# Performance work log

Measured on AMD Instinct MI355X. Metric: run time of the kernel, lower is better.

Reference implementation:

```python
import jax, jax.numpy as jnp
import numpy as np

E, K, H, I, T, CAP = 32, 4, 2048, 2048, 512, 256
ALPHA, LIMIT = 1.702, 7.0


def _dyn_quant(x):
    # symmetric per-token int8 dynamic quant (npu_dynamic_quant): dequant = q * scale
    s = jnp.max(jnp.abs(x), axis=-1, keepdims=True) / 127.0
    q = jnp.clip(jnp.round(x / s), -127.0, 127.0)  # int8 values kept in f32 for exact-emulated GEMM
    return q, jnp.squeeze(s, -1)


def _swiglu(x):
    glu = jnp.minimum(x[..., ::2], LIMIT)          # interleaved layout, upper clamp only
    lin = jnp.clip(x[..., 1::2], -LIMIT, LIMIT)
    return glu * jax.nn.sigmoid(ALPHA * glu) * (lin + 1.0)


def _forward(hidden_states, router_logits, gate_up_proj, gate_up_proj_scale,
             gate_up_proj_bias, down_proj, down_proj_scale, down_proj_bias):
    # --- gating: softmax + top-k, renormalize weights (npu_moe_gating_top_k + explicit renorm) ---
    probs = jax.nn.softmax(router_logits, axis=-1)
    topk_w, topk_ids = jax.lax.top_k(probs, K)                     # [T,K]
    topk_w = topk_w / jnp.sum(topk_w, axis=-1, keepdims=True)
    # --- per-token dynamic int8 quant of activations ---
    q_x, x_scale = _dyn_quant(hidden_states)                        # [T,H], [T]
    # --- capacity-based dispatch (emulates npu_moe_init_routing_v2 sort/scatter) ---
    flat_e = topk_ids.reshape(-1)                                   # [T*K]
    tok = jnp.repeat(jnp.arange(T), K)
    oh = jax.nn.one_hot(flat_e, E, dtype=jnp.int32)
    pos = jnp.take_along_axis(jnp.cumsum(oh, axis=0) - 1, flat_e[:, None], axis=1)[:, 0]
    valid = pos < CAP
    x_disp = jnp.zeros((E, CAP, H), jnp.float32).at[flat_e, pos].set(q_x[tok], mode='drop')
    s_disp = jnp.zeros((E, CAP), jnp.float32).at[flat_e, pos].set(x_scale[tok], mode='drop')
    gu = jnp.einsum('ech,ehf->ecf', x_disp, gate_up_proj.astype(jnp.float32))
    gu = gu * s_disp[:, :, None] * gate_up_proj_scale[:, None, :] + gate_up_proj_bias[:, None, :]
    act = _swiglu(gu)                                               # [E,CAP,I]
    # --- requantize + grouped GEMM 2 + bias ---
    q2, s2 = _dyn_quant(act)
    dn = jnp.einsum('eci,eio->eco', q2, down_proj.astype(jnp.float32))
    dn = dn * s2[:, :, None] * down_proj_scale[:, None, :] + down_proj_bias[:, None, :]
    # --- finalize routing: gather back and weighted combine ---
    pos_c = jnp.minimum(pos, CAP - 1)
    y = dn[flat_e, pos_c] * valid[:, None].astype(jnp.float32)      # [T*K,H]
    return jnp.sum(y.reshape(T, K, H) * topk_w[:, :, None], axis=1)


def setup_inputs() -> dict:
    key = jax.random.key(0)
    k = jax.random.split(key, 8)
    hidden_states = jax.random.normal(k[0], (T, H), jnp.float32)
    router_logits = jax.random.normal(k[1], (T, E), jnp.float32)
    gate_up_proj = jax.random.randint(k[2], (E, H, 2 * I), -127, 128, jnp.int32).astype(jnp.int8)
    w_s = float(2.0 / (127.0 * np.sqrt(H)))
    gate_up_proj_scale = (0.5 + 0.5 * jax.random.uniform(k[3], (E, 2 * I), jnp.float32)) * w_s
    gate_up_proj_bias = 0.02 * jax.random.normal(k[4], (E, 2 * I), jnp.float32)
    down_proj = jax.random.randint(k[5], (E, I, H), -127, 128, jnp.int32).astype(jnp.int8)
    d_s = float(2.0 / (127.0 * np.sqrt(I)))
    down_proj_scale = (0.5 + 0.5 * jax.random.uniform(k[6], (E, H), jnp.float32)) * d_s
    down_proj_bias = 0.02 * jax.random.normal(k[7], (E, H), jnp.float32)
    return dict(hidden_states=hidden_states, router_logits=router_logits,
                gate_up_proj=gate_up_proj, gate_up_proj_scale=gate_up_proj_scale,
                gate_up_proj_bias=gate_up_proj_bias, down_proj=down_proj,
                down_proj_scale=down_proj_scale, down_proj_bias=down_proj_bias)


def reference(hidden_states, router_logits, gate_up_proj, gate_up_proj_scale,
              gate_up_proj_bias, down_proj, down_proj_scale, down_proj_bias):
    return _forward(hidden_states, router_logits, gate_up_proj, gate_up_proj_scale,
                    gate_up_proj_bias, down_proj, down_proj_scale, down_proj_bias)
```

## Files before the change

### kernel.cpp

```cpp
#include <hip/hip_runtime.h>
#include <hip/hip_bf16.h>
#include <math.h>

constexpr int E_EXP = 32;
constexpr int TOPK  = 4;
constexpr int H_DIM = 2048;
constexpr int I_DIM = 2048;
constexpr int T_TOK = 512;
constexpr int CAP   = 256;
constexpr int TWOI  = 4096;
constexpr int NPAIR = T_TOK * TOPK;
constexpr float ALPHA = 1.702f;
constexpr float LIMIT = 7.0f;


typedef int v4i  __attribute__((ext_vector_type(4)));
typedef int v16i __attribute__((ext_vector_type(16)));

__device__ __forceinline__ float waveReduceMax(float v) {
    #pragma unroll
    for (int off = 32; off > 0; off >>= 1)
        v = fmaxf(v, __shfl_xor(v, off, 64));
    return v;
}

__global__ void k_router(const float* __restrict__ logits,
                         int* __restrict__ topk_ids,
                         float* __restrict__ topk_w) {
    int t = blockIdx.x * blockDim.x + threadIdx.x;
    if (t >= T_TOK) return;
    float l[E_EXP];
    float mx = -1e30f;
    #pragma unroll
    for (int e = 0; e < E_EXP; e++) { l[e] = logits[t * E_EXP + e]; mx = fmaxf(mx, l[e]); }
    #pragma unroll
    for (int e = 0; e < E_EXP; e++) { l[e] = expf(l[e] - mx); }

    float v[TOPK]; int id[TOPK];
    #pragma unroll
    for (int k = 0; k < TOPK; k++) {
        float best = -1.0f; int bi = 0;
        #pragma unroll
        for (int e = 0; e < E_EXP; e++) {
            bool taken = false;
            for (int j = 0; j < k; j++) taken = taken || (id[j] == e);
            if (!taken && l[e] > best) { best = l[e]; bi = e; }
        }
        v[k] = best; id[k] = bi;
    }
    float inv = 1.0f / (v[0] + v[1] + v[2] + v[3]);
    #pragma unroll
    for (int k = 0; k < TOPK; k++) {
        topk_ids[t * TOPK + k] = id[k];
        topk_w[t * TOPK + k]   = v[k] * inv;
    }
}

__global__ void k_quant_x(const float* __restrict__ x,
                          signed char* __restrict__ qx,
                          float* __restrict__ xs) {
    int t = blockIdx.x, tid = threadIdx.x;
    const float4* xr = (const float4*)(x + (size_t)t * H_DIM);
    float4 v0 = xr[tid * 2], v1 = xr[tid * 2 + 1];
    float am = fmaxf(fmaxf(fmaxf(fabsf(v0.x), fabsf(v0.y)), fmaxf(fabsf(v0.z), fabsf(v0.w))),
                     fmaxf(fmaxf(fabsf(v1.x), fabsf(v1.y)), fmaxf(fabsf(v1.z), fabsf(v1.w))));
    __shared__ float red[4];
    am = waveReduceMax(am);
    if ((tid & 63) == 0) red[tid >> 6] = am;
    __syncthreads();
    am = fmaxf(fmaxf(red[0], red[1]), fmaxf(red[2], red[3]));
    float s = am * (1.0f / 127.0f);
    if (tid == 0) xs[t] = s;
    float vv[8] = {v0.x, v0.y, v0.z, v0.w, v1.x, v1.y, v1.z, v1.w};
    int out[2]; signed char* ob = (signed char*)out;
    #pragma unroll
    for (int j = 0; j < 8; j++) {
        float q = (s > 0.f) ? rintf(vv[j] / s) : 0.f;
        q = fminf(127.f, fmaxf(-127.f, q));
        ob[j] = (signed char)q;
    }
    ((int2*)(qx + (size_t)t * H_DIM))[tid] = *(int2*)out;
}

__global__ void k_dispatch(const int* __restrict__ topk_ids,
                           int* __restrict__ pair_pos,
                           int* __restrict__ rows_map,
                           int* __restrict__ counts) {
    int e = blockIdx.x;
    int lane = threadIdx.x;
    int base = 0;
    unsigned long long lt = (1ull << lane) - 1ull;
    if (lane == 63) lt = 0x7FFFFFFFFFFFFFFFull;
    for (int i0 = 0; i0 < NPAIR; i0 += 64) {
        int idx = i0 + lane;
        int ee = topk_ids[idx];
        bool m = (ee == e);
        unsigned long long mask = __ballot(m);
        int pre = __popcll(mask & lt);
        if (m) {
            int pos = base + pre;
            pair_pos[idx] = pos;
            if (pos < CAP) rows_map[e * CAP + pos] = idx;
        }
        base += __popcll(mask);
    }
    if (lane == 0) counts[e] = (base < CAP) ? base : CAP;
}

__global__ void k_scan(const int* __restrict__ counts, int* __restrict__ offs) {
    if (threadIdx.x == 0 && blockIdx.x == 0) {
        int a = 0;
        for (int e = 0; e < E_EXP; e++) { offs[e] = a; a += counts[e]; }
        offs[E_EXP] = a;
    }
}

#define MT 128
#define NT 64
#define KC 64
#define LSTR 80

__global__ __launch_bounds__(256, 4) void k_gemm1(
    const signed char* __restrict__ qx, const float* __restrict__ xs,
    const int* __restrict__ W, const float* __restrict__ wscale,
    const float* __restrict__ wbias, const int* __restrict__ rows_map,
    const int* __restrict__ counts, const int* __restrict__ offs,
    float* __restrict__ act) {
    int e = blockIdx.z;
    int cnt = counts[e];
    int m0 = blockIdx.y * MT;
    if (m0 >= cnt) return;
    int rb = offs[e];
    int n0 = blockIdx.x * NT;
    int tid = threadIdx.x;

    __shared__ __align__(16) signed char a_lds[MT * LSTR];
    __shared__ __align__(16) signed char b_lds[NT * LSTR];
    __shared__ int   asrc_lds[MT];
    __shared__ float s_lds[MT];

    if (tid < MT) {
        int r = m0 + tid;
        int tok = 0; float sc = 0.f;
        if (r < cnt) { int pair = rows_map[e * CAP + r]; tok = pair >> 2; sc = xs[tok]; }
        asrc_lds[tid] = tok; s_lds[tid] = sc;
    }
    __syncthreads();

    int arow = tid >> 2, ahalf = tid & 3;
    const signed char* ap0 = qx + (size_t)asrc_lds[arow]      * H_DIM + ahalf * 16;
    const signed char* ap1 = qx + (size_t)asrc_lds[arow + 64] * H_DIM + ahalf * 16;
    signed char* aw0 = a_lds + arow * LSTR + ahalf * 16;
    signed char* aw1 = a_lds + (arow + 64) * LSTR + ahalf * 16;

    int nq = tid & 15, kq = tid >> 4;
    const int* bp = W + (size_t)e * H_DIM * TWOI + (size_t)(kq * 4) * TWOI + n0 + nq * 4;
    int* bw = (int*)(b_lds + (nq * 4) * LSTR) + kq;

    int lane = tid & 63, wv = tid >> 6;
    int wr = wv >> 1, wc = wv & 1;
    int l31 = lane & 31, lhi = lane >> 5;
    const signed char* ar = a_lds + (wr * 64 + l31) * LSTR + lhi * 16;
    const signed char* br = b_lds + (wc * 32 + l31) * LSTR + lhi * 16;

    v16i acc0 = {}, acc1 = {};

    for (int k0 = 0; k0 < H_DIM; k0 += KC) {
        int4 va0 = *(const int4*)ap0;
        int4 va1 = *(const int4*)ap1;
        int4 w0 = *(const int4*)(bp);
        int4 w1 = *(const int4*)(bp + TWOI);
        int4 w2 = *(const int4*)(bp + 2 * TWOI);
        int4 w3 = *(const int4*)(bp + 3 * TWOI);
        ap0 += KC; ap1 += KC; bp += (size_t)KC * TWOI;

        *(int4*)aw0 = va0;
        *(int4*)aw1 = va1;
        bw[0]      = (w0.x & 255) | ((w1.x & 255) << 8) | ((w2.x & 255) << 16) | (w3.x << 24);
        bw[20]     = (w0.y & 255) | ((w1.y & 255) << 8) | ((w2.y & 255) << 16) | (w3.y << 24);
        bw[40]     = (w0.z & 255) | ((w1.z & 255) << 8) | ((w2.z & 255) << 16) | (w3.z << 24);
        bw[60]     = (w0.w & 255) | ((w1.w & 255) << 8) | ((w2.w & 255) << 16) | (w3.w << 24);
        __syncthreads();

        #pragma unroll
        for (int kk = 0; kk < 2; kk++) {
            v4i bf = *(const v4i*)(br + kk * 32);
            v4i a0 = *(const v4i*)(ar + kk * 32);
            v4i a1 = *(const v4i*)(ar + 32 * LSTR + kk * 32);
            acc0 = __builtin_amdgcn_mfma_i32_32x32x32_i8(a0, bf, acc0, 0, 0, 0);
            acc1 = __builtin_amdgcn_mfma_i32_32x32x32_i8(a1, bf, acc1, 0, 0, 0);
        }
        __syncthreads();
    }

    int c = n0 + wc * 32 + l31;
    float wsc = wscale[e * TWOI + c];
    float wbs = wbias[e * TWOI + c];
    bool evenc = (l31 & 1) == 0;
    #pragma unroll
    for (int i = 0; i < 2; i++) {
        #pragma unroll
        for (int reg = 0; reg < 16; reg++) {
            int row_local = wr * 64 + i * 32 + (reg & 3) + 8 * (reg >> 2) + 4 * lhi;
            int accv = (i == 0) ? acc0[reg] : acc1[reg];
            float val = (float)accv * s_lds[row_local] * wsc + wbs;
            float other = __shfl_xor(val, 1, 64);
            int r = m0 + row_local;
            if (evenc && r < cnt) {
                float g   = fminf(val, LIMIT);
                float lin = fminf(fmaxf(other, -LIMIT), LIMIT);
                float sig = 1.0f / (1.0f + expf(-ALPHA * g));
                act[(size_t)(rb + r) * I_DIM + (c >> 1)] = g * sig * (lin + 1.0f);
            }
        }
    }
}

__global__ void k_quant_act(const float* __restrict__ act,
                            const int* __restrict__ counts,
                            const int* __restrict__ offs,
                            signed char* __restrict__ aq,
                            float* __restrict__ as_) {
    int e = blockIdx.x / CAP, p = blockIdx.x % CAP;
    if (p >= counts[e]) return;
    int row = offs[e] + p;
    int tid = threadIdx.x;
    const float4* xr = (const float4*)(act + (size_t)row * I_DIM);
    float4 v0 = xr[tid * 2], v1 = xr[tid * 2 + 1];
    float am = fmaxf(fmaxf(fmaxf(fabsf(v0.x), fabsf(v0.y)), fmaxf(fabsf(v0.z), fabsf(v0.w))),
                     fmaxf(fmaxf(fabsf(v1.x), fabsf(v1.y)), fmaxf(fabsf(v1.z), fabsf(v1.w))));
    __shared__ float red[4];
    am = waveReduceMax(am);
    if ((tid & 63) == 0) red[tid >> 6] = am;
    __syncthreads();
    am = fmaxf(fmaxf(red[0], red[1]), fmaxf(red[2], red[3]));
    float s = am * (1.0f / 127.0f);
    if (tid == 0) as_[row] = s;
    float vv[8] = {v0.x, v0.y, v0.z, v0.w, v1.x, v1.y, v1.z, v1.w};
    int out[2]; signed char* ob = (signed char*)out;
    #pragma unroll
    for (int j = 0; j < 8; j++) {
        float q = (s > 0.f) ? rintf(vv[j] / s) : 0.f;
        q = fminf(127.f, fmaxf(-127.f, q));
        ob[j] = (signed char)q;
    }
    ((int2*)(aq + (size_t)row * I_DIM))[tid] = *(int2*)out;
}

__global__ __launch_bounds__(256, 4) void k_gemm2(
    const signed char* __restrict__ aq, const float* __restrict__ as_,
    const int* __restrict__ W, const float* __restrict__ wscale,
    const float* __restrict__ wbias, const int* __restrict__ rows_map,
    const int* __restrict__ counts, const int* __restrict__ offs,
    float* __restrict__ dn_rows) {
    int e = blockIdx.z;
    int cnt = counts[e];
    int m0 = blockIdx.y * MT;
    if (m0 >= cnt) return;
    int rb = offs[e];
    int n0 = blockIdx.x * NT;
    int tid = threadIdx.x;

    __shared__ __align__(16) signed char a_lds[MT * LSTR];
    __shared__ __align__(16) signed char b_lds[NT * LSTR];
    __shared__ int   asrc_lds[MT];
    __shared__ int   pair_lds[MT];
    __shared__ float s_lds[MT];

    if (tid < MT) {
        int r = m0 + tid;
        int src = rb; int pr = 0; float sc = 0.f;
        if (r < cnt) { src = rb + r; pr = rows_map[e * CAP + r]; sc = as_[rb + r]; }
        asrc_lds[tid] = src; pair_lds[tid] = pr; s_lds[tid] = sc;
    }
    __syncthreads();

    int arow = tid >> 2, ahalf = tid & 3;
    const signed char* ap0 = aq + (size_t)asrc_lds[arow]      * I_DIM + ahalf * 16;
    const signed char* ap1 = aq + (size_t)asrc_lds[arow + 64] * I_DIM + ahalf * 16;
    signed char* aw0 = a_lds + arow * LSTR + ahalf * 16;
    signed char* aw1 = a_lds + (arow + 64) * LSTR + ahalf * 16;

    int nq = tid & 15, kq = tid >> 4;
    const int* bp = W + (size_t)e * I_DIM * H_DIM + (size_t)(kq * 4) * H_DIM + n0 + nq * 4;
    int* bw = (int*)(b_lds + (nq * 4) * LSTR) + kq;

    int lane = tid & 63, wv = tid >> 6;
    int wr = wv >> 1, wc = wv & 1;
    int l31 = lane & 31, lhi = lane >> 5;
    const signed char* ar = a_lds + (wr * 64 + l31) * LSTR + lhi * 16;
    const signed char* br = b_lds + (wc * 32 + l31) * LSTR + lhi * 16;

    v16i acc0 = {}, acc1 = {};

    for (int k0 = 0; k0 < I_DIM; k0 += KC) {
        int4 va0 = *(const int4*)ap0;
        int4 va1 = *(const int4*)ap1;
        int4 w0 = *(const int4*)(bp);
        int4 w1 = *(const int4*)(bp + H_DIM);
        int4 w2 = *(const int4*)(bp + 2 * H_DIM);
        int4 w3 = *(const int4*)(bp + 3 * H_DIM);
        ap0 += KC; ap1 += KC; bp += (size_t)KC * H_DIM;

        *(int4*)aw0 = va0;
        *(int4*)aw1 = va1;
        bw[0]  = (w0.x & 255) | ((w1.x & 255) << 8) | ((w2.x & 255) << 16) | (w3.x << 24);
        bw[20] = (w0.y & 255) | ((w1.y & 255) << 8) | ((w2.y & 255) << 16) | (w3.y << 24);
        bw[40] = (w0.z & 255) | ((w1.z & 255) << 8) | ((w2.z & 255) << 16) | (w3.z << 24);
        bw[60] = (w0.w & 255) | ((w1.w & 255) << 8) | ((w2.w & 255) << 16) | (w3.w << 24);
        __syncthreads();

        #pragma unroll
        for (int kk = 0; kk < 2; kk++) {
            v4i bf = *(const v4i*)(br + kk * 32);
            v4i a0 = *(const v4i*)(ar + kk * 32);
            v4i a1 = *(const v4i*)(ar + 32 * LSTR + kk * 32);
            acc0 = __builtin_amdgcn_mfma_i32_32x32x32_i8(a0, bf, acc0, 0, 0, 0);
            acc1 = __builtin_amdgcn_mfma_i32_32x32x32_i8(a1, bf, acc1, 0, 0, 0);
        }
        __syncthreads();
    }

    int c = n0 + wc * 32 + l31;
    float wsc = wscale[e * H_DIM + c];
    float wbs = wbias[e * H_DIM + c];
    #pragma unroll
    for (int i = 0; i < 2; i++) {
        #pragma unroll
        for (int reg = 0; reg < 16; reg++) {
            int row_local = wr * 64 + i * 32 + (reg & 3) + 8 * (reg >> 2) + 4 * lhi;
            int r = m0 + row_local;
            if (r < cnt) {
                int accv = (i == 0) ? acc0[reg] : acc1[reg];
                float val = (float)accv * s_lds[row_local] * wsc + wbs;
                dn_rows[(size_t)pair_lds[row_local] * H_DIM + c] = val;
            }
        }
    }
}

__global__ void k_finalize(const float* __restrict__ dn_rows,
                           const float* __restrict__ topk_w,
                           const int* __restrict__ pair_pos,
                           float* __restrict__ out) {
    int t = blockIdx.x, tid = threadIdx.x;
    int h = tid * 8;
    float acc[8] = {0, 0, 0, 0, 0, 0, 0, 0};
    #pragma unroll
    for (int k = 0; k < TOPK; k++) {
        int pair = t * TOPK + k;
        if (pair_pos[pair] < CAP) {
            float w = topk_w[pair];
            const float4* dr = (const float4*)(dn_rows + (size_t)pair * H_DIM + h);
            float4 d0 = dr[0], d1 = dr[1];
            acc[0] += w * d0.x; acc[1] += w * d0.y; acc[2] += w * d0.z; acc[3] += w * d0.w;
            acc[4] += w * d1.x; acc[5] += w * d1.y; acc[6] += w * d1.z; acc[7] += w * d1.w;
        }
    }
    float4* o = (float4*)(out + (size_t)t * H_DIM + h);
    o[0] = make_float4(acc[0], acc[1], acc[2], acc[3]);
    o[1] = make_float4(acc[4], acc[5], acc[6], acc[7]);
}

extern "C" void kernel_launch(void* const* d_in, const int* in_sizes, int n_in,
                              void* d_out, int out_size, void* d_ws, size_t ws_size,
                              hipStream_t stream) {
    const float* hidden  = (const float*)d_in[0];
    const float* rlogits = (const float*)d_in[1];
    const int*   gup     = (const int*)d_in[2];
    const float* gup_s   = (const float*)d_in[3];
    const float* gup_b   = (const float*)d_in[4];
    const int*   dnw     = (const int*)d_in[5];
    const float* dn_s    = (const float*)d_in[6];
    const float* dn_b    = (const float*)d_in[7];
    float*       out     = (float*)d_out;

    char* ws = (char*)d_ws;
    size_t off = 0;
    auto alloc = [&](size_t bytes) -> void* {
        void* p = ws + off;
        off = (off + bytes + 255) & ~(size_t)255;
        return p;
    };
    signed char* qx       = (signed char*)alloc((size_t)T_TOK * H_DIM);
    float*       xs       = (float*)alloc((size_t)T_TOK * 4);
    int*         topk_ids = (int*)alloc((size_t)NPAIR * 4);
    float*       topk_w   = (float*)alloc((size_t)NPAIR * 4);
    int*         pair_pos = (int*)alloc((size_t)NPAIR * 4);
    int*         rows_map = (int*)alloc((size_t)E_EXP * CAP * 4);
    int*         counts   = (int*)alloc((size_t)E_EXP * 4);
    int*         offs     = (int*)alloc((size_t)(E_EXP + 1) * 4);
    float*       act      = (float*)alloc((size_t)NPAIR * I_DIM * 4);
    signed char* aq       = (signed char*)alloc((size_t)NPAIR * I_DIM);
    float*       as_      = (float*)alloc((size_t)NPAIR * 4);
    float*       dnr      = (float*)alloc((size_t)NPAIR * H_DIM * 4);

    k_router<<<dim3((T_TOK + 255) / 256), dim3(256), 0, stream>>>(rlogits, topk_ids, topk_w);
    k_quant_x<<<dim3(T_TOK), dim3(256), 0, stream>>>(hidden, qx, xs);
    k_dispatch<<<dim3(E_EXP), dim3(64), 0, stream>>>(topk_ids, pair_pos, rows_map, counts);
    k_scan<<<dim3(1), dim3(64), 0, stream>>>(counts, offs);
    k_gemm1<<<dim3(TWOI / NT, CAP / MT, E_EXP), dim3(256), 0, stream>>>(
        qx, xs, gup, gup_s, gup_b, rows_map, counts, offs, act);
    k_quant_act<<<dim3(E_EXP * CAP), dim3(256), 0, stream>>>(act, counts, offs, aq, as_);
    k_gemm2<<<dim3(H_DIM / NT, CAP / MT, E_EXP), dim3(256), 0, stream>>>(
        aq, as_, dnw, dn_s, dn_b, rows_map, counts, offs, dnr);
    k_finalize<<<dim3(T_TOK), dim3(256), 0, stream>>>(dnr, topk_w, pair_pos, out);
}
```

Measured before the change: 1.745 ms.

## Double-buffer LDS tiles with register prefetch and swizzled layouts in MoE GEMMs

```diff
diff --git a/kernel.cpp b/kernel.cpp
--- a/kernel.cpp
+++ b/kernel.cpp
@@ -118,7 +118,7 @@
 #define MT 128
 #define NT 64
 #define KC 64
-#define LSTR 80
+#define ASTR 80
 
 __global__ __launch_bounds__(256, 4) void k_gemm1(
     const signed char* __restrict__ qx, const float* __restrict__ xs,
@@ -134,61 +134,89 @@
     int n0 = blockIdx.x * NT;
     int tid = threadIdx.x;
 
-    __shared__ __align__(16) signed char a_lds[MT * LSTR];
-    __shared__ __align__(16) signed char b_lds[NT * LSTR];
-    __shared__ int   asrc_lds[MT];
+    __shared__ __align__(16) signed char a_sm[2][MT * ASTR];
+    __shared__ __align__(16) int b_sm[2][16 * 64];
+    __shared__ int   tok_lds[MT];
     __shared__ float s_lds[MT];
 
     if (tid < MT) {
         int r = m0 + tid;
         int tok = 0; float sc = 0.f;
         if (r < cnt) { int pair = rows_map[e * CAP + r]; tok = pair >> 2; sc = xs[tok]; }
-        asrc_lds[tid] = tok; s_lds[tid] = sc;
+        tok_lds[tid] = tok; s_lds[tid] = sc;
     }
     __syncthreads();
 
     int arow = tid >> 2, ahalf = tid & 3;
-    const signed char* ap0 = qx + (size_t)asrc_lds[arow]      * H_DIM + ahalf * 16;
-    const signed char* ap1 = qx + (size_t)asrc_lds[arow + 64] * H_DIM + ahalf * 16;
-    signed char* aw0 = a_lds + arow * LSTR + ahalf * 16;
-    signed char* aw1 = a_lds + (arow + 64) * LSTR + ahalf * 16;
+    const signed char* ap0 = qx + (size_t)tok_lds[arow]      * H_DIM + ahalf * 16;
+    const signed char* ap1 = qx + (size_t)tok_lds[arow + 64] * H_DIM + ahalf * 16;
+    int aw_off  = arow * ASTR + ((ahalf ^ ((arow >> 3) & 3)) << 4);
+    int aw_off1 = aw_off + 64 * ASTR;
 
     int nq = tid & 15, kq = tid >> 4;
     const int* bp = W + (size_t)e * H_DIM * TWOI + (size_t)(kq * 4) * TWOI + n0 + nq * 4;
-    int* bw = (int*)(b_lds + (nq * 4) * LSTR) + kq;
+    int bw_woff = kq * 64 + nq * 4;
 
     int lane = tid & 63, wv = tid >> 6;
     int wr = wv >> 1, wc = wv & 1;
     int l31 = lane & 31, lhi = lane >> 5;
-    const signed char* ar = a_lds + (wr * 64 + l31) * LSTR + lhi * 16;
-    const signed char* br = b_lds + (wc * 32 + l31) * LSTR + lhi * 16;
+    int qz = (l31 >> 3) & 3;
+    int ar_off  = (wr * 64 + l31) * ASTR;
+    int c_off0 = ((lhi) ^ qz) << 4;
+    int c_off1 = ((lhi + 2) ^ qz) << 4;
+    int br_woff = 256 * lhi + wc * 32 + l31;
 
     v16i acc0 = {}, acc1 = {};
 
-    for (int k0 = 0; k0 < H_DIM; k0 += KC) {
-        int4 va0 = *(const int4*)ap0;
-        int4 va1 = *(const int4*)ap1;
-        int4 w0 = *(const int4*)(bp);
-        int4 w1 = *(const int4*)(bp + TWOI);
-        int4 w2 = *(const int4*)(bp + 2 * TWOI);
-        int4 w3 = *(const int4*)(bp + 3 * TWOI);
-        ap0 += KC; ap1 += KC; bp += (size_t)KC * TWOI;
-
-        *(int4*)aw0 = va0;
-        *(int4*)aw1 = va1;
-        bw[0]      = (w0.x & 255) | ((w1.x & 255) << 8) | ((w2.x & 255) << 16) | (w3.x << 24);
-        bw[20]     = (w0.y & 255) | ((w1.y & 255) << 8) | ((w2.y & 255) << 16) | (w3.y << 24);
-        bw[40]     = (w0.z & 255) | ((w1.z & 255) << 8) | ((w2.z & 255) << 16) | (w3.z << 24);
-        bw[60]     = (w0.w & 255) | ((w1.w & 255) << 8) | ((w2.w & 255) << 16) | (w3.w << 24);
-        __syncthreads();
-
+    int4 va0 = *(const int4*)ap0, va1 = *(const int4*)ap1;
+    int4 wv0 = *(const int4*)(bp);
+    int4 wv1 = *(const int4*)(bp + TWOI);
+    int4 wv2 = *(const int4*)(bp + 2 * TWOI);
+    int4 wv3 = *(const int4*)(bp + 3 * TWOI);
+    ap0 += KC; ap1 += KC; bp += (size_t)KC * TWOI;
+    *(int4*)(a_sm[0] + aw_off)  = va0;
+    *(int4*)(a_sm[0] + aw_off1) = va1;
+    {
+        v4i pk = { (wv0.x & 255) | ((wv1.x & 255) << 8) | ((wv2.x & 255) << 16) | (wv3.x << 24),
+                   (wv0.y & 255) | ((wv1.y & 255) << 8) | ((wv2.y & 255) << 16) | (wv3.y << 24),
+                   (wv0.z & 255) | ((wv1.z & 255) << 8) | ((wv2.z & 255) << 16) | (wv3.z << 24),
+                   (wv0.w & 255) | ((wv1.w & 255) << 8) | ((wv2.w & 255) << 16) | (wv3.w << 24) };
+        *(v4i*)(b_sm[0] + bw_woff) = pk;
+    }
+    __syncthreads();
+
+    constexpr int NSTEP = H_DIM / KC;
+    for (int t = 0; t < NSTEP; ++t) {
+        int cur = t & 1;
+        bool more = (t + 1 < NSTEP);
+        if (more) {
+            va0 = *(const int4*)ap0; va1 = *(const int4*)ap1;
+            wv0 = *(const int4*)(bp);
+            wv1 = *(const int4*)(bp + TWOI);
+            wv2 = *(const int4*)(bp + 2 * TWOI);
+            wv3 = *(const int4*)(bp + 3 * TWOI);
+            ap0 += KC; ap1 += KC; bp += (size_t)KC * TWOI;
+        }
+        const signed char* aA = a_sm[cur] + ar_off;
+        const int* bB = b_sm[cur] + br_woff;
         #pragma unroll
-        for (int kk = 0; kk < 2; kk++) {
-            v4i bf = *(const v4i*)(br + kk * 32);
-            v4i a0 = *(const v4i*)(ar + kk * 32);
-            v4i a1 = *(const v4i*)(ar + 32 * LSTR + kk * 32);
+        for (int kk = 0; kk < 2; ++kk) {
+            int coff = kk ? c_off1 : c_off0;
+            v4i a0 = *(const v4i*)(aA + coff);
+            v4i a1 = *(const v4i*)(aA + 32 * ASTR + coff);
+            v4i bf = { bB[512 * kk], bB[512 * kk + 64], bB[512 * kk + 128], bB[512 * kk + 192] };
             acc0 = __builtin_amdgcn_mfma_i32_32x32x32_i8(a0, bf, acc0, 0, 0, 0);
             acc1 = __builtin_amdgcn_mfma_i32_32x32x32_i8(a1, bf, acc1, 0, 0, 0);
+        }
+        if (more) {
+            int nb = cur ^ 1;
+            *(int4*)(a_sm[nb] + aw_off)  = va0;
+            *(int4*)(a_sm[nb] + aw_off1) = va1;
+            v4i pk = { (wv0.x & 255) | ((wv1.x & 255) << 8) | ((wv2.x & 255) << 16) | (wv3.x << 24),
+                       (wv0.y & 255) | ((wv1.y & 255) << 8) | ((wv2.y & 255) << 16) | (wv3.y << 24),
+                       (wv0.z & 255) | ((wv1.z & 255) << 8) | ((wv2.z & 255) << 16) | (wv3.z << 24),
+                       (wv0.w & 255) | ((wv1.w & 255) << 8) | ((wv2.w & 255) << 16) | (wv3.w << 24) };
+            *(v4i*)(b_sm[nb] + bw_woff) = pk;
         }
         __syncthreads();
     }
@@ -261,9 +289,9 @@
     int n0 = blockIdx.x * NT;
     int tid = threadIdx.x;
 
-    __shared__ __align__(16) signed char a_lds[MT * LSTR];
-    __shared__ __align__(16) signed char b_lds[NT * LSTR];
-    __shared__ int   asrc_lds[MT];
+    __shared__ __align__(16) signed char a_sm[2][MT * ASTR];
+    __shared__ __align__(16) int b_sm[2][16 * 64];
+    __shared__ int   src_lds[MT];
     __shared__ int   pair_lds[MT];
     __shared__ float s_lds[MT];
 
@@ -271,52 +299,80 @@
         int r = m0 + tid;
         int src = rb; int pr = 0; float sc = 0.f;
         if (r < cnt) { src = rb + r; pr = rows_map[e * CAP + r]; sc = as_[rb + r]; }
-        asrc_lds[tid] = src; pair_lds[tid] = pr; s_lds[tid] = sc;
+        src_lds[tid] = src; pair_lds[tid] = pr; s_lds[tid] = sc;
     }
     __syncthreads();
 
     int arow = tid >> 2, ahalf = tid & 3;
-    const signed char* ap0 = aq + (size_t)asrc_lds[arow]      * I_DIM + ahalf * 16;
-    const signed char* ap1 = aq + (size_t)asrc_lds[arow + 64] * I_DIM + ahalf * 16;
-    signed char* aw0 = a_lds + arow * LSTR + ahalf * 16;
-    signed char* aw1 = a_lds + (arow + 64) * LSTR + ahalf * 16;
+    const signed char* ap0 = aq + (size_t)src_lds[arow]      * I_DIM + ahalf * 16;
+    const signed char* ap1 = aq + (size_t)src_lds[arow + 64] * I_DIM + ahalf * 16;
+    int aw_off  = arow * ASTR + ((ahalf ^ ((arow >> 3) & 3)) << 4);
+    int aw_off1 = aw_off + 64 * ASTR;
 
     int nq = tid & 15, kq = tid >> 4;
     const int* bp = W + (size_t)e * I_DIM * H_DIM + (size_t)(kq * 4) * H_DIM + n0 + nq * 4;
-    int* bw = (int*)(b_lds + (nq * 4) * LSTR) + kq;
+    int bw_woff = kq * 64 + nq * 4;
 
     int lane = tid & 63, wv = tid >> 6;
     int wr = wv >> 1, wc = wv & 1;
     int l31 = lane & 31, lhi = lane >> 5;
-    const signed char* ar = a_lds + (wr * 64 + l31) * LSTR + lhi * 16;
-    const signed char* br = b_lds + (wc * 32 + l31) * LSTR + lhi * 16;
+    int qz = (l31 >> 3) & 3;
+    int ar_off  = (wr * 64 + l31) * ASTR;
+    int c_off0 = ((lhi) ^ qz) << 4;
+    int c_off1 = ((lhi + 2) ^ qz) << 4;
+    int br_woff = 256 * lhi + wc * 32 + l31;
 
     v16i acc0 = {}, acc1 = {};
 
-    for (int k0 = 0; k0 < I_DIM; k0 += KC) {
-        int4 va0 = *(const int4*)ap0;
-        int4 va1 = *(const int4*)ap1;
-        int4 w0 = *(const int4*)(bp);
-        int4 w1 = *(const int4*)(bp + H_DIM);
-        int4 w2 = *(const int4*)(bp + 2 * H_DIM);
-        int4 w3 = *(const int4*)(bp + 3 * H_DIM);
-        ap0 += KC; ap1 += KC; bp += (size_t)KC * H_DIM;
-
-        *(int4*)aw0 = va0;
-        *(int4*)aw1 = va1;
-        bw[0]  = (w0.x & 255) | ((w1.x & 255) << 8) | ((w2.x & 255) << 16) | (w3.x << 24);
-        bw[20] = (w0.y & 255) | ((w1.y & 255) << 8) | ((w2.y & 255) << 16) | (w3.y << 24);
-        bw[40] = (w0.z & 255) | ((w1.z & 255) << 8) | ((w2.z & 255) << 16) | (w3.z << 24);
-        bw[60] = (w0.w & 255) | ((w1.w & 255) << 8) | ((w2.w & 255) << 16) | (w3.w << 24);
-        __syncthreads();
-
+    int4 va0 = *(const int4*)ap0, va1 = *(const int4*)ap1;
+    int4 wv0 = *(const int4*)(bp);
+    int4 wv1 = *(const int4*)(bp + H_DIM);
+    int4 wv2 = *(const int4*)(bp + 2 * H_DIM);
+    int4 wv3 = *(const int4*)(bp + 3 * H_DIM);
+    ap0 += KC; ap1 += KC; bp += (size_t)KC * H_DIM;
+    *(int4*)(a_sm[0] + aw_off)  = va0;
+    *(int4*)(a_sm[0] + aw_off1) = va1;
+    {
+        v4i pk = { (wv0.x & 255) | ((wv1.x & 255) << 8) | ((wv2.x & 255) << 16) | (wv3.x << 24),
+                   (wv0.y & 255) | ((wv1.y & 255) << 8) | ((wv2.y & 255) << 16) | (wv3.y << 24),
+                   (wv0.z & 255) | ((wv1.z & 255) << 8) | ((wv2.z & 255) << 16) | (wv3.z << 24),
+                   (wv0.w & 255) | ((wv1.w & 255) << 8) | ((wv2.w & 255) << 16) | (wv3.w << 24) };
+        *(v4i*)(b_sm[0] + bw_woff) = pk;
+    }
+    __syncthreads();
+
+    constexpr int NSTEP = I_DIM / KC;
+    for (int t = 0; t < NSTEP; ++t) {
+        int cur = t & 1;
+        bool more = (t + 1 < NSTEP);
+        if (more) {
+            va0 = *(const int4*)ap0; va1 = *(const int4*)ap1;
+            wv0 = *(const int4*)(bp);
+            wv1 = *(const int4*)(bp + H_DIM);
+            wv2 = *(const int4*)(bp + 2 * H_DIM);
+            wv3 = *(const int4*)(bp + 3 * H_DIM);
+            ap0 += KC; ap1 += KC; bp += (size_t)KC * H_DIM;
+        }
+        const signed char* aA = a_sm[cur] + ar_off;
+        const int* bB = b_sm[cur] + br_woff;
         #pragma unroll
-        for (int kk = 0; kk < 2; kk++) {
-            v4i bf = *(const v4i*)(br + kk * 32);
-            v4i a0 = *(const v4i*)(ar + kk * 32);
-            v4i a1 = *(const v4i*)(ar + 32 * LSTR + kk * 32);
+        for (int kk = 0; kk < 2; ++kk) {
+            int coff = kk ? c_off1 : c_off0;
+            v4i a0 = *(const v4i*)(aA + coff);
+            v4i a1 = *(const v4i*)(aA + 32 * ASTR + coff);
+            v4i bf = { bB[512 * kk], bB[512 * kk + 64], bB[512 * kk + 128], bB[512 * kk + 192] };
             acc0 = __builtin_amdgcn_mfma_i32_32x32x32_i8(a0, bf, acc0, 0, 0, 0);
             acc1 = __builtin_amdgcn_mfma_i32_32x32x32_i8(a1, bf, acc1, 0, 0, 0);
+        }
+        if (more) {
+            int nb = cur ^ 1;
+            *(int4*)(a_sm[nb] + aw_off)  = va0;
+            *(int4*)(a_sm[nb] + aw_off1) = va1;
+            v4i pk = { (wv0.x & 255) | ((wv1.x & 255) << 8) | ((wv2.x & 255) << 16) | (wv3.x << 24),
+                       (wv0.y & 255) | ((wv1.y & 255) << 8) | ((wv2.y & 255) << 16) | (wv3.y << 24),
+                       (wv0.z & 255) | ((wv1.z & 255) << 8) | ((wv2.z & 255) << 16) | (wv3.z << 24),
+                       (wv0.w & 255) | ((wv1.w & 255) << 8) | ((wv2.w & 255) << 16) | (wv3.w << 24) };
+            *(v4i*)(b_sm[nb] + bw_woff) = pk;
         }
         __syncthreads();
     }
```

Measured after the change: 1.741 ms. Within noise of the previous version (-0.2%).
